# Kernel optimization log

Measured on AMD Instinct MI355X. Metric: run time of the kernel, lower is better.

## Reference

```python
import jax, jax.numpy as jnp
import numpy as np

N_NODES = 50000
N_EDGES = 800000
IN_C, H0, H1, OUT_C = 64, 64, 64, 16
EPS = 1e-5


def _sage_min(x, src, dst, Wl, bl, Wr, n_nodes):
    # PyG SAGEConv(aggr='min'): out = lin_l(min_{j in N(i)} x_j) + lin_r(x_i)
    agg = jax.ops.segment_min(x[src], dst, num_segments=n_nodes)
    agg = jnp.where(jnp.isfinite(agg), agg, 0.0)  # empty segments -> 0 (torch_scatter default)
    return agg @ Wl + bl + x @ Wr


def _batchnorm(x, gamma, beta):
    # training-mode BatchNorm1d over node dim, biased variance, eps=1e-5
    mu = jnp.mean(x, axis=0)
    var = jnp.mean((x - mu) ** 2, axis=0)
    return gamma * (x - mu) * jax.lax.rsqrt(var + EPS) + beta


def setup_inputs() -> dict:
    key = jax.random.key(0)
    ks = jax.random.split(key, 16)
    x = jax.random.normal(ks[0], (N_NODES, IN_C), dtype=jnp.float32)
    edge_index = jax.random.randint(ks[1], (2, N_EDGES), 0, N_NODES, dtype=jnp.int64)

    def lin(k, fan_in, fan_out):
        s = 1.0 / np.sqrt(fan_in)
        return jax.random.uniform(k, (fan_in, fan_out), jnp.float32, -s, s)

    return {
        "x": x, "edge_index": edge_index,
        "W1l": lin(ks[2], IN_C, H0), "b1": jnp.zeros((H0,), jnp.float32), "W1r": lin(ks[3], IN_C, H0),
        "g1": jnp.ones((H0,), jnp.float32), "be1": jnp.zeros((H0,), jnp.float32),
        "W2l": lin(ks[4], H0, H1), "b2": jnp.zeros((H1,), jnp.float32), "W2r": lin(ks[5], H0, H1),
        "g2": jnp.ones((H1,), jnp.float32), "be2": jnp.zeros((H1,), jnp.float32),
        "W3l": lin(ks[6], H1, OUT_C), "b3": jnp.zeros((OUT_C,), jnp.float32), "W3r": lin(ks[7], H1, OUT_C),
    }


def reference(x, edge_index, W1l, b1, W1r, g1, be1, W2l, b2, W2r, g2, be2, W3l, b3, W3r):
    src, dst = edge_index[0], edge_index[1]
    n = x.shape[0]
    h = jax.nn.relu(_batchnorm(_sage_min(x, src, dst, W1l, b1, W1r, n), g1, be1))
    h = jax.nn.relu(_batchnorm(_sage_min(h, src, dst, W2l, b2, W2r, n), g2, be2))
    h = _sage_min(h, src, dst, W3l, b3, W3r, n)
    return jax.nn.log_softmax(h, axis=1)
```

## Files before the change

kernel.cpp:

```cpp
#include <hip/hip_runtime.h>
#include <stdint.h>


#define NG 8

__device__ __forceinline__ float bnrelu1(float v, float mu, float is, float g, float b) {
    return fmaxf((v - mu) * is * g + b, 0.0f);
}

__global__ __launch_bounds__(256)
void k_prep(int* __restrict__ deg, int n_nodes, const int* __restrict__ ei32,
            int* __restrict__ flag) {
    int i = blockIdx.x * blockDim.x + threadIdx.x;
    int stride = gridDim.x * blockDim.x;
    for (int j = i; j < n_nodes; j += stride) deg[j] = 0;
    if (i == 0) {
        int allzero = 1;
        for (int t = 1; t < 32; t += 2) allzero &= (ei32[t] == 0);
        *flag = allzero;
    }
}

__global__ __launch_bounds__(256)
void k_convert(const void* __restrict__ ei, int n_edges,
               const int* __restrict__ flag, int* __restrict__ src32,
               int* __restrict__ dst32) {
    const bool is64 = (*flag != 0);
    const int* e32 = (const int*)ei;
    const long long* e64 = (const long long*)ei;
    int i = blockIdx.x * blockDim.x + threadIdx.x;
    int stride = gridDim.x * blockDim.x;
    for (int e = i; e < n_edges; e += stride) {
        if (is64) { src32[e] = (int)e64[e]; dst32[e] = (int)e64[n_edges + e]; }
        else      { src32[e] = e32[e];      dst32[e] = e32[n_edges + e]; }
    }
}

__global__ __launch_bounds__(256)
void k_hist_r(const int* __restrict__ dst32, int n_edges, int* __restrict__ deg,
              int NN, int blocks_per_group) {
    const int g = blockIdx.x & (NG - 1);
    const int jb = blockIdx.x >> 3;
    const int lo = (int)((long long)g * NN / NG);
    const int hi = (int)((long long)(g + 1) * NN / NG);
    const int stride = blocks_per_group * 256;
    for (int e = jb * 256 + threadIdx.x; e < n_edges; e += stride) {
        int d = dst32[e];
        if (d >= lo && d < hi) atomicAdd(&deg[d], 1);
    }
}

__global__ __launch_bounds__(256)
void k_scan1(const int* __restrict__ deg, int* __restrict__ bsum, int n) {
    __shared__ int red[256];
    const int t = threadIdx.x;
    const int i = blockIdx.x * 256 + t;
    red[t] = (i < n) ? deg[i] : 0;
    __syncthreads();
    for (int off = 128; off; off >>= 1) {
        if (t < off) red[t] += red[t + off];
        __syncthreads();
    }
    if (t == 0) bsum[blockIdx.x] = red[0];
}

__global__ __launch_bounds__(1024)
void k_scan2(const int* __restrict__ bsum, int* __restrict__ boffs,
             int nb, int* __restrict__ rowptr, int n) {
    __shared__ int part[1024];
    const int t = threadIdx.x;
    part[t] = (t < nb) ? bsum[t] : 0;
    __syncthreads();
    for (int off = 1; off < 1024; off <<= 1) {
        int v = (t >= off) ? part[t - off] : 0;
        __syncthreads();
        part[t] += v;
        __syncthreads();
    }
    if (t < nb) boffs[t] = (t == 0) ? 0 : part[t - 1];
    if (t == 0) rowptr[n] = part[nb - 1];
}

__global__ __launch_bounds__(256)
void k_scan3(const int* __restrict__ deg, const int* __restrict__ boffs,
             int* __restrict__ rowptr, int* __restrict__ cursor, int n) {
    __shared__ int part[256];
    const int t = threadIdx.x;
    const int i = blockIdx.x * 256 + t;
    const int d = (i < n) ? deg[i] : 0;
    part[t] = d;
    __syncthreads();
    for (int off = 1; off < 256; off <<= 1) {
        int v = (t >= off) ? part[t - off] : 0;
        __syncthreads();
        part[t] += v;
        __syncthreads();
    }
    if (i < n) {
        int excl = boffs[blockIdx.x] + part[t] - d;
        rowptr[i] = excl;
        cursor[i] = excl;
    }
}

__global__ __launch_bounds__(256)
void k_fill_r(const int* __restrict__ src32, const int* __restrict__ dst32,
              int n_edges, int* __restrict__ cursor, int* __restrict__ csr,
              int NN, int blocks_per_group) {
    const int g = blockIdx.x & (NG - 1);
    const int jb = blockIdx.x >> 3;
    const int lo = (int)((long long)g * NN / NG);
    const int hi = (int)((long long)(g + 1) * NN / NG);
    const int stride = blocks_per_group * 256;
    for (int e = jb * 256 + threadIdx.x; e < n_edges; e += stride) {
        int d = dst32[e];
        if (d >= lo && d < hi) {
            int pos = atomicAdd(&cursor[d], 1);
            csr[pos] = src32[e];
        }
    }
}

template <bool BN>
__global__ __launch_bounds__(256)
void k_agg(const float* __restrict__ x, const int* __restrict__ rowptr,
           const int* __restrict__ csr, float* __restrict__ agg, int NN,
           const float* __restrict__ mu, const float* __restrict__ istd,
           const float* __restrict__ gam, const float* __restrict__ bet) {
    const int lane = threadIdx.x & 63;
    const int wave = (blockIdx.x * blockDim.x + threadIdx.x) >> 6;
    const int nwaves = (gridDim.x * blockDim.x) >> 6;
    float s_mu = 0.f, s_is = 0.f, s_g = 0.f, s_b = 0.f;
    if (BN) { s_mu = mu[lane]; s_is = istd[lane]; s_g = gam[lane]; s_b = bet[lane]; }
    for (int n = wave; n < NN; n += nwaves) {
        const int beg = rowptr[n], end = rowptr[n + 1];
        float m = __builtin_inff();
        int e = beg;
        for (; e + 4 <= end; e += 4) {
            int s0 = csr[e], s1 = csr[e + 1], s2 = csr[e + 2], s3 = csr[e + 3];
            float v0 = x[(size_t)s0 * 64 + lane];
            float v1 = x[(size_t)s1 * 64 + lane];
            float v2 = x[(size_t)s2 * 64 + lane];
            float v3 = x[(size_t)s3 * 64 + lane];
            if (BN) {
                v0 = bnrelu1(v0, s_mu, s_is, s_g, s_b);
                v1 = bnrelu1(v1, s_mu, s_is, s_g, s_b);
                v2 = bnrelu1(v2, s_mu, s_is, s_g, s_b);
                v3 = bnrelu1(v3, s_mu, s_is, s_g, s_b);
            }
            m = fminf(m, fminf(fminf(v0, v1), fminf(v2, v3)));
        }
        for (; e < end; ++e) {
            float v = x[(size_t)csr[e] * 64 + lane];
            if (BN) v = bnrelu1(v, s_mu, s_is, s_g, s_b);
            m = fminf(m, v);
        }
        agg[(size_t)n * 64 + lane] = (end > beg) ? m : 0.0f;
    }
}

template <bool BNX>
__global__ __launch_bounds__(256)
void k_gemm64(const float* __restrict__ agg, const float* __restrict__ xin,
              const float* __restrict__ Wl, const float* __restrict__ bl,
              const float* __restrict__ Wr, float* __restrict__ hout,
              double* __restrict__ psum, double* __restrict__ psq, int n_nodes,
              const float* __restrict__ mu, const float* __restrict__ istd,
              const float* __restrict__ gam, const float* __restrict__ bet) {
    __shared__ float sWl[64][64];
    __shared__ float sWr[64][64];
    __shared__ float rowA[4][64];
    __shared__ float rowX[4][64];
    __shared__ double red[4][64];
    const int t = threadIdx.x, c = t & 63, ln = t >> 6;
    for (int i = t; i < 4096; i += 256) {
        ((float*)sWl)[i] = Wl[i];
        ((float*)sWr)[i] = Wr[i];
    }
    float s_mu = 0.f, s_is = 0.f, s_g = 0.f, s_b = 0.f;
    if (BNX) { s_mu = mu[c]; s_is = istd[c]; s_g = gam[c]; s_b = bet[c]; }
    const float bc = bl[c];
    double lsum = 0.0, lsq = 0.0;
    const int nchunk = (n_nodes + 3) >> 2;
    for (int chunk = blockIdx.x; chunk < nchunk; chunk += gridDim.x) {
        const int node = chunk * 4 + ln;
        __syncthreads();
        if (node < n_nodes) {
            rowA[ln][c] = agg[(size_t)node * 64 + c];
            float v = xin[(size_t)node * 64 + c];
            if (BNX) v = bnrelu1(v, s_mu, s_is, s_g, s_b);
            rowX[ln][c] = v;
        }
        __syncthreads();
        if (node < n_nodes) {
            float acc = bc;
#pragma unroll
            for (int k = 0; k < 64; ++k)
                acc = fmaf(rowA[ln][k], sWl[k][c], fmaf(rowX[ln][k], sWr[k][c], acc));
            hout[(size_t)node * 64 + c] = acc;
            lsum += (double)acc;
            lsq  += (double)acc * (double)acc;
        }
    }
    __syncthreads();
    red[ln][c] = lsum;
    __syncthreads();
    if (ln == 0)
        psum[(size_t)blockIdx.x * 64 + c] = red[0][c] + red[1][c] + red[2][c] + red[3][c];
    __syncthreads();
    red[ln][c] = lsq;
    __syncthreads();
    if (ln == 0)
        psq[(size_t)blockIdx.x * 64 + c] = red[0][c] + red[1][c] + red[2][c] + red[3][c];
}

__global__ __launch_bounds__(1024)
void k_finalize(const double* __restrict__ psum, const double* __restrict__ psq,
                float* __restrict__ mu, float* __restrict__ istd,
                int n_nodes, int nblocks) {
    __shared__ double s_s[16][64];
    __shared__ double s_q[16][64];
    const int t = threadIdx.x;
    const int c = t & 63, g = t >> 6;
    double s = 0.0, q = 0.0;
    for (int b = g; b < nblocks; b += 16) {
        s += psum[(size_t)b * 64 + c];
        q += psq[(size_t)b * 64 + c];
    }
    s_s[g][c] = s;
    s_q[g][c] = q;
    __syncthreads();
    if (g == 0) {
        double S = 0.0, Q = 0.0;
#pragma unroll
        for (int i = 0; i < 16; ++i) { S += s_s[i][c]; Q += s_q[i][c]; }
        double m = S / n_nodes;
        double var = Q / n_nodes - m * m;
        mu[c] = (float)m;
        istd[c] = (float)(1.0 / sqrt(var + 1e-5));
    }
}

__global__ __launch_bounds__(256)
void k_l3(const float* __restrict__ agg, const float* __restrict__ xin,
          const float* __restrict__ W3l, const float* __restrict__ b3,
          const float* __restrict__ W3r, float* __restrict__ out, int n_nodes,
          const float* __restrict__ mu, const float* __restrict__ istd,
          const float* __restrict__ gam, const float* __restrict__ bet) {
    __shared__ float sWl[64][16];
    __shared__ float sWr[64][16];
    __shared__ float rowA[16][65];
    __shared__ float rowX[16][65];
    const int t = threadIdx.x;
    for (int i = t; i < 1024; i += 256) {
        ((float*)sWl)[i] = W3l[i];
        ((float*)sWr)[i] = W3r[i];
    }
    const int kc = t & 63;
    const float s_mu = mu[kc], s_is = istd[kc], s_g = gam[kc], s_b = bet[kc];
    const int base = blockIdx.x * 16;
#pragma unroll
    for (int i = 0; i < 4; ++i) {
        int j = t + i * 256;
        int nd = j >> 6, k = j & 63;
        int gnode = base + nd;
        if (gnode < n_nodes) {
            rowA[nd][k] = agg[(size_t)gnode * 64 + k];
            rowX[nd][k] = bnrelu1(xin[(size_t)gnode * 64 + k], s_mu, s_is, s_g, s_b);
        } else {
            rowA[nd][k] = 0.0f;
            rowX[nd][k] = 0.0f;
        }
    }
    __syncthreads();
    const int n = t >> 4, c = t & 15;
    float acc = b3[c];
#pragma unroll
    for (int k = 0; k < 64; ++k)
        acc = fmaf(rowA[n][k], sWl[k][c], fmaf(rowX[n][k], sWr[k][c], acc));
    float m = acc;
    for (int off = 8; off; off >>= 1) m = fmaxf(m, __shfl_xor(m, off, 16));
    float ex = expf(acc - m);
    float ssum = ex;
    for (int off = 8; off; off >>= 1) ssum += __shfl_xor(ssum, off, 16);
    if (base + n < n_nodes)
        out[(size_t)(base + n) * 16 + c] = (acc - m) - logf(ssum);
}

extern "C" void kernel_launch(void* const* d_in, const int* in_sizes, int n_in,
                              void* d_out, int out_size, void* d_ws, size_t ws_size,
                              hipStream_t stream) {
    (void)n_in; (void)out_size; (void)ws_size;
    const float* x   = (const float*)d_in[0];
    const void*  ei  = d_in[1];
    const float* W1l = (const float*)d_in[2];
    const float* b1  = (const float*)d_in[3];
    const float* W1r = (const float*)d_in[4];
    const float* g1  = (const float*)d_in[5];
    const float* be1 = (const float*)d_in[6];
    const float* W2l = (const float*)d_in[7];
    const float* b2  = (const float*)d_in[8];
    const float* W2r = (const float*)d_in[9];
    const float* g2  = (const float*)d_in[10];
    const float* be2 = (const float*)d_in[11];
    const float* W3l = (const float*)d_in[12];
    const float* b3  = (const float*)d_in[13];
    const float* W3r = (const float*)d_in[14];
    float* out = (float*)d_out;

    const int NN = in_sizes[0] / 64;
    const int n_edges = in_sizes[1] / 2;
    const int nAgg = NN * 64;

    size_t off = 0;
    auto alloc = [&](size_t bytes) {
        void* p = (char*)d_ws + off;
        off = (off + bytes + 255) & ~(size_t)255;
        return p;
    };
    float* agg    = (float*)alloc((size_t)nAgg * 4);
    float* hA     = (float*)alloc((size_t)nAgg * 4);
    float* hB     = (float*)alloc((size_t)nAgg * 4);
    int*   csr    = (int*)  alloc((size_t)n_edges * 4);
    int*   src32  = (int*)  alloc((size_t)n_edges * 4);
    int*   dst32  = (int*)  alloc((size_t)n_edges * 4);
    int*   rowptr = (int*)  alloc((size_t)(NN + 1) * 4);
    int*   cursor = (int*)  alloc((size_t)NN * 4);
    int*   deg    = (int*)  alloc((size_t)NN * 4);
    int*   bsum   = (int*)  alloc(1024 * 4);
    int*   boffs  = (int*)  alloc(1024 * 4);
    const int GG = 512;
    double* psum  = (double*)alloc((size_t)GG * 64 * 8);
    double* psq   = (double*)alloc((size_t)GG * 64 * 8);
    float*  mu1   = (float*) alloc(64 * 4);
    float*  istd1 = (float*) alloc(64 * 4);
    float*  mu2   = (float*) alloc(64 * 4);
    float*  istd2 = (float*) alloc(64 * 4);
    int*    flag  = (int*)   alloc(4);

    const int GHF = 1024;
    const int BPG = GHF / NG;
    const int NB = (NN + 255) / 256;
    const int GA = 2048;
    const int GL3 = (NN + 15) / 16;

    k_prep   <<<256, 256, 0, stream>>>(deg, NN, (const int*)ei, flag);
    k_convert<<<1024, 256, 0, stream>>>(ei, n_edges, flag, src32, dst32);
    k_hist_r <<<GHF, 256, 0, stream>>>(dst32, n_edges, deg, NN, BPG);
    k_scan1  <<<NB, 256, 0, stream>>>(deg, bsum, NN);
    k_scan2  <<<1, 1024, 0, stream>>>(bsum, boffs, NB, rowptr, NN);
    k_scan3  <<<NB, 256, 0, stream>>>(deg, boffs, rowptr, cursor, NN);
    k_fill_r <<<GHF, 256, 0, stream>>>(src32, dst32, n_edges, cursor, csr, NN, BPG);

    k_agg<false><<<GA, 256, 0, stream>>>(x, rowptr, csr, agg, NN,
                                         nullptr, nullptr, nullptr, nullptr);
    k_gemm64<false><<<GG, 256, 0, stream>>>(agg, x, W1l, b1, W1r, hA, psum, psq, NN,
                                            nullptr, nullptr, nullptr, nullptr);
    k_finalize<<<1, 1024, 0, stream>>>(psum, psq, mu1, istd1, NN, GG);
    k_agg<true><<<GA, 256, 0, stream>>>(hA, rowptr, csr, agg, NN, mu1, istd1, g1, be1);
    k_gemm64<true><<<GG, 256, 0, stream>>>(agg, hA, W2l, b2, W2r, hB, psum, psq, NN,
                                           mu1, istd1, g1, be1);
    k_finalize<<<1, 1024, 0, stream>>>(psum, psq, mu2, istd2, NN, GG);
    k_agg<true><<<GA, 256, 0, stream>>>(hB, rowptr, csr, agg, NN, mu2, istd2, g2, be2);
    k_l3<<<GL3, 256, 0, stream>>>(agg, hB, W3l, b3, W3r, out, NN, mu2, istd2, g2, be2);
}
```

Baseline: 404.6 us.

## Fuse min-aggregation with per-node linear layers and merge histogram into conversion

Merges the gather-min aggregation and the dense Wl/Wr projection into a single per-layer kernel. Each wave aggregates one node, stages the row in shared memory, and multiplies it against weights held in registers. This removes the intermediate agg buffer round-trip and several launches, and the final layer is fused the same way including log-softmax. The degree histogram is folded into the index-conversion kernel with plain global atomics, dropping the grouped pass. BN partial sums move from double to float accumulation, and the 128 weight registers per thread may limit occupancy.

```diff
diff --git a/kernel.cpp b/kernel.cpp
--- a/kernel.cpp
+++ b/kernel.cpp
@@ -22,31 +22,21 @@
 }
 
 __global__ __launch_bounds__(256)
-void k_convert(const void* __restrict__ ei, int n_edges,
-               const int* __restrict__ flag, int* __restrict__ src32,
-               int* __restrict__ dst32) {
+void k_convert_hist(const void* __restrict__ ei, int n_edges,
+                    const int* __restrict__ flag, int* __restrict__ src32,
+                    int* __restrict__ dst32, int* __restrict__ deg) {
     const bool is64 = (*flag != 0);
     const int* e32 = (const int*)ei;
     const long long* e64 = (const long long*)ei;
     int i = blockIdx.x * blockDim.x + threadIdx.x;
     int stride = gridDim.x * blockDim.x;
     for (int e = i; e < n_edges; e += stride) {
-        if (is64) { src32[e] = (int)e64[e]; dst32[e] = (int)e64[n_edges + e]; }
-        else      { src32[e] = e32[e];      dst32[e] = e32[n_edges + e]; }
-    }
-}
-
-__global__ __launch_bounds__(256)
-void k_hist_r(const int* __restrict__ dst32, int n_edges, int* __restrict__ deg,
-              int NN, int blocks_per_group) {
-    const int g = blockIdx.x & (NG - 1);
-    const int jb = blockIdx.x >> 3;
-    const int lo = (int)((long long)g * NN / NG);
-    const int hi = (int)((long long)(g + 1) * NN / NG);
-    const int stride = blocks_per_group * 256;
-    for (int e = jb * 256 + threadIdx.x; e < n_edges; e += stride) {
-        int d = dst32[e];
-        if (d >= lo && d < hi) atomicAdd(&deg[d], 1);
+        int s, d;
+        if (is64) { s = (int)e64[e]; d = (int)e64[n_edges + e]; }
+        else      { s = e32[e];      d = e32[n_edges + e]; }
+        src32[e] = s;
+        dst32[e] = d;
+        atomicAdd(&deg[d], 1);
     }
 }
 
@@ -122,100 +112,105 @@
 }
 
 template <bool BN>
-__global__ __launch_bounds__(256)
-void k_agg(const float* __restrict__ x, const int* __restrict__ rowptr,
-           const int* __restrict__ csr, float* __restrict__ agg, int NN,
-           const float* __restrict__ mu, const float* __restrict__ istd,
-           const float* __restrict__ gam, const float* __restrict__ bet) {
-    const int lane = threadIdx.x & 63;
-    const int wave = (blockIdx.x * blockDim.x + threadIdx.x) >> 6;
-    const int nwaves = (gridDim.x * blockDim.x) >> 6;
+__global__ __launch_bounds__(256, 2)
+void k_layer(const float* __restrict__ xin, const int* __restrict__ rowptr,
+             const int* __restrict__ csr, const float* __restrict__ Wl,
+             const float* __restrict__ bl, const float* __restrict__ Wr,
+             float* __restrict__ hout, float* __restrict__ psum,
+             float* __restrict__ psq, int NN,
+             const float* __restrict__ mu, const float* __restrict__ istd,
+             const float* __restrict__ gam, const float* __restrict__ bet) {
+    __shared__ float rowA[4][64];
+    __shared__ float rowX[4][64];
+    __shared__ float red[4][64];
+    const int t = threadIdx.x, lane = t & 63, w = t >> 6;
+    float wl[64], wr[64];
+#pragma unroll
+    for (int k = 0; k < 64; ++k) {
+        wl[k] = Wl[k * 64 + lane];
+        wr[k] = Wr[k * 64 + lane];
+    }
     float s_mu = 0.f, s_is = 0.f, s_g = 0.f, s_b = 0.f;
     if (BN) { s_mu = mu[lane]; s_is = istd[lane]; s_g = gam[lane]; s_b = bet[lane]; }
+    const float bc = bl[lane];
+    float lsum = 0.f, lsq = 0.f;
+    const int wave = blockIdx.x * 4 + w;
+    const int nwaves = gridDim.x * 4;
     for (int n = wave; n < NN; n += nwaves) {
         const int beg = rowptr[n], end = rowptr[n + 1];
         float m = __builtin_inff();
         int e = beg;
-        for (; e + 4 <= end; e += 4) {
+        for (; e + 8 <= end; e += 8) {
             int s0 = csr[e], s1 = csr[e + 1], s2 = csr[e + 2], s3 = csr[e + 3];
-            float v0 = x[(size_t)s0 * 64 + lane];
-            float v1 = x[(size_t)s1 * 64 + lane];
-            float v2 = x[(size_t)s2 * 64 + lane];
-            float v3 = x[(size_t)s3 * 64 + lane];
+            int s4 = csr[e + 4], s5 = csr[e + 5], s6 = csr[e + 6], s7 = csr[e + 7];
+            float v0 = xin[(size_t)s0 * 64 + lane];
+            float v1 = xin[(size_t)s1 * 64 + lane];
+            float v2 = xin[(size_t)s2 * 64 + lane];
+            float v3 = xin[(size_t)s3 * 64 + lane];
+            float v4 = xin[(size_t)s4 * 64 + lane];
+            float v5 = xin[(size_t)s5 * 64 + lane];
+            float v6 = xin[(size_t)s6 * 64 + lane];
+            float v7 = xin[(size_t)s7 * 64 + lane];
             if (BN) {
                 v0 = bnrelu1(v0, s_mu, s_is, s_g, s_b);
                 v1 = bnrelu1(v1, s_mu, s_is, s_g, s_b);
                 v2 = bnrelu1(v2, s_mu, s_is, s_g, s_b);
                 v3 = bnrelu1(v3, s_mu, s_is, s_g, s_b);
+                v4 = bnrelu1(v4, s_mu, s_is, s_g, s_b);
+                v5 = bnrelu1(v5, s_mu, s_is, s_g, s_b);
+                v6 = bnrelu1(v6, s_mu, s_is, s_g, s_b);
+                v7 = bnrelu1(v7, s_mu, s_is, s_g, s_b);
             }
-            m = fminf(m, fminf(fminf(v0, v1), fminf(v2, v3)));
+            m = fminf(m, fminf(fminf(fminf(v0, v1), fminf(v2, v3)),
+                               fminf(fminf(v4, v5), fminf(v6, v7))));
         }
         for (; e < end; ++e) {
-            float v = x[(size_t)csr[e] * 64 + lane];
+            float v = xin[(size_t)csr[e] * 64 + lane];
             if (BN) v = bnrelu1(v, s_mu, s_is, s_g, s_b);
             m = fminf(m, v);
         }
-        agg[(size_t)n * 64 + lane] = (end > beg) ? m : 0.0f;
-    }
-}
-
-template <bool BNX>
-__global__ __launch_bounds__(256)
-void k_gemm64(const float* __restrict__ agg, const float* __restrict__ xin,
-              const float* __restrict__ Wl, const float* __restrict__ bl,
-              const float* __restrict__ Wr, float* __restrict__ hout,
-              double* __restrict__ psum, double* __restrict__ psq, int n_nodes,
-              const float* __restrict__ mu, const float* __restrict__ istd,
-              const float* __restrict__ gam, const float* __restrict__ bet) {
-    __shared__ float sWl[64][64];
-    __shared__ float sWr[64][64];
-    __shared__ float rowA[4][64];
-    __shared__ float rowX[4][64];
-    __shared__ double red[4][64];
-    const int t = threadIdx.x, c = t & 63, ln = t >> 6;
-    for (int i = t; i < 4096; i += 256) {
-        ((float*)sWl)[i] = Wl[i];
-        ((float*)sWr)[i] = Wr[i];
-    }
-    float s_mu = 0.f, s_is = 0.f, s_g = 0.f, s_b = 0.f;
-    if (BNX) { s_mu = mu[c]; s_is = istd[c]; s_g = gam[c]; s_b = bet[c]; }
-    const float bc = bl[c];
-    double lsum = 0.0, lsq = 0.0;
-    const int nchunk = (n_nodes + 3) >> 2;
-    for (int chunk = blockIdx.x; chunk < nchunk; chunk += gridDim.x) {
-        const int node = chunk * 4 + ln;
-        __syncthreads();
-        if (node < n_nodes) {
-            rowA[ln][c] = agg[(size_t)node * 64 + c];
-            float v = xin[(size_t)node * 64 + c];
-            if (BNX) v = bnrelu1(v, s_mu, s_is, s_g, s_b);
-            rowX[ln][c] = v;
-        }
-        __syncthreads();
-        if (node < n_nodes) {
-            float acc = bc;
-#pragma unroll
-            for (int k = 0; k < 64; ++k)
-                acc = fmaf(rowA[ln][k], sWl[k][c], fmaf(rowX[ln][k], sWr[k][c], acc));
-            hout[(size_t)node * 64 + c] = acc;
-            lsum += (double)acc;
-            lsq  += (double)acc * (double)acc;
-        }
-    }
-    __syncthreads();
-    red[ln][c] = lsum;
-    __syncthreads();
-    if (ln == 0)
-        psum[(size_t)blockIdx.x * 64 + c] = red[0][c] + red[1][c] + red[2][c] + red[3][c];
-    __syncthreads();
-    red[ln][c] = lsq;
-    __syncthreads();
-    if (ln == 0)
-        psq[(size_t)blockIdx.x * 64 + c] = red[0][c] + red[1][c] + red[2][c] + red[3][c];
+        const float av = (end > beg) ? m : 0.0f;
+        float xv = xin[(size_t)n * 64 + lane];
+        if (BN) xv = bnrelu1(xv, s_mu, s_is, s_g, s_b);
+        rowA[w][lane] = av;
+        rowX[w][lane] = xv;
+        asm volatile("s_waitcnt lgkmcnt(0)" ::: "memory");
+        __builtin_amdgcn_sched_barrier(0);
+        float a0 = 0.f, a1 = 0.f, a2 = 0.f, a3 = 0.f;
+#pragma unroll
+        for (int k4 = 0; k4 < 16; ++k4) {
+            const float4 a4 = *(const float4*)&rowA[w][k4 * 4];
+            const float4 x4 = *(const float4*)&rowX[w][k4 * 4];
+            a0 = fmaf(a4.x, wl[k4 * 4 + 0], a0);
+            a1 = fmaf(a4.y, wl[k4 * 4 + 1], a1);
+            a2 = fmaf(a4.z, wl[k4 * 4 + 2], a2);
+            a3 = fmaf(a4.w, wl[k4 * 4 + 3], a3);
+            a0 = fmaf(x4.x, wr[k4 * 4 + 0], a0);
+            a1 = fmaf(x4.y, wr[k4 * 4 + 1], a1);
+            a2 = fmaf(x4.z, wr[k4 * 4 + 2], a2);
+            a3 = fmaf(x4.w, wr[k4 * 4 + 3], a3);
+        }
+        const float h = bc + ((a0 + a1) + (a2 + a3));
+        hout[(size_t)n * 64 + lane] = h;
+        lsum += h;
+        lsq = fmaf(h, h, lsq);
+    }
+    __syncthreads();
+    red[w][lane] = lsum;
+    __syncthreads();
+    if (w == 0)
+        psum[(size_t)blockIdx.x * 64 + lane] =
+            red[0][lane] + red[1][lane] + red[2][lane] + red[3][lane];
+    __syncthreads();
+    red[w][lane] = lsq;
+    __syncthreads();
+    if (w == 0)
+        psq[(size_t)blockIdx.x * 64 + lane] =
+            red[0][lane] + red[1][lane] + red[2][lane] + red[3][lane];
 }
 
 __global__ __launch_bounds__(1024)
-void k_finalize(const double* __restrict__ psum, const double* __restrict__ psq,
+void k_finalize(const float* __restrict__ psum, const float* __restrict__ psq,
                 float* __restrict__ mu, float* __restrict__ istd,
                 int n_nodes, int nblocks) {
     __shared__ double s_s[16][64];
@@ -224,8 +219,8 @@
     const int c = t & 63, g = t >> 6;
     double s = 0.0, q = 0.0;
     for (int b = g; b < nblocks; b += 16) {
-        s += psum[(size_t)b * 64 + c];
-        q += psq[(size_t)b * 64 + c];
+        s += (double)psum[(size_t)b * 64 + c];
+        q += (double)psq[(size_t)b * 64 + c];
     }
     s_s[g][c] = s;
     s_q[g][c] = q;
@@ -241,50 +236,76 @@
     }
 }
 
-__global__ __launch_bounds__(256)
-void k_l3(const float* __restrict__ agg, const float* __restrict__ xin,
-          const float* __restrict__ W3l, const float* __restrict__ b3,
-          const float* __restrict__ W3r, float* __restrict__ out, int n_nodes,
-          const float* __restrict__ mu, const float* __restrict__ istd,
-          const float* __restrict__ gam, const float* __restrict__ bet) {
-    __shared__ float sWl[64][16];
-    __shared__ float sWr[64][16];
-    __shared__ float rowA[16][65];
-    __shared__ float rowX[16][65];
-    const int t = threadIdx.x;
-    for (int i = t; i < 1024; i += 256) {
-        ((float*)sWl)[i] = W3l[i];
-        ((float*)sWr)[i] = W3r[i];
-    }
-    const int kc = t & 63;
-    const float s_mu = mu[kc], s_is = istd[kc], s_g = gam[kc], s_b = bet[kc];
-    const int base = blockIdx.x * 16;
-#pragma unroll
-    for (int i = 0; i < 4; ++i) {
-        int j = t + i * 256;
-        int nd = j >> 6, k = j & 63;
-        int gnode = base + nd;
-        if (gnode < n_nodes) {
-            rowA[nd][k] = agg[(size_t)gnode * 64 + k];
-            rowX[nd][k] = bnrelu1(xin[(size_t)gnode * 64 + k], s_mu, s_is, s_g, s_b);
-        } else {
-            rowA[nd][k] = 0.0f;
-            rowX[nd][k] = 0.0f;
-        }
-    }
-    __syncthreads();
-    const int n = t >> 4, c = t & 15;
-    float acc = b3[c];
-#pragma unroll
-    for (int k = 0; k < 64; ++k)
-        acc = fmaf(rowA[n][k], sWl[k][c], fmaf(rowX[n][k], sWr[k][c], acc));
-    float m = acc;
-    for (int off = 8; off; off >>= 1) m = fmaxf(m, __shfl_xor(m, off, 16));
-    float ex = expf(acc - m);
-    float ssum = ex;
-    for (int off = 8; off; off >>= 1) ssum += __shfl_xor(ssum, off, 16);
-    if (base + n < n_nodes)
-        out[(size_t)(base + n) * 16 + c] = (acc - m) - logf(ssum);
+__global__ __launch_bounds__(256, 2)
+void k_layer3(const float* __restrict__ xin, const int* __restrict__ rowptr,
+              const int* __restrict__ csr, const float* __restrict__ W3l,
+              const float* __restrict__ b3, const float* __restrict__ W3r,
+              float* __restrict__ out, int NN,
+              const float* __restrict__ mu, const float* __restrict__ istd,
+              const float* __restrict__ gam, const float* __restrict__ bet) {
+    __shared__ float rowA[4][64];
+    __shared__ float rowX[4][64];
+    const int t = threadIdx.x, lane = t & 63, w = t >> 6;
+    const int c = lane & 15, q = lane >> 4;
+    float wl3[16], wr3[16];
+#pragma unroll
+    for (int j = 0; j < 16; ++j) {
+        wl3[j] = W3l[(q * 16 + j) * 16 + c];
+        wr3[j] = W3r[(q * 16 + j) * 16 + c];
+    }
+    const float s_mu = mu[lane], s_is = istd[lane], s_g = gam[lane], s_b = bet[lane];
+    const float bc = b3[c];
+    const int wave = blockIdx.x * 4 + w;
+    const int nwaves = gridDim.x * 4;
+    for (int n = wave; n < NN; n += nwaves) {
+        const int beg = rowptr[n], end = rowptr[n + 1];
+        float m = __builtin_inff();
+        int e = beg;
+        for (; e + 8 <= end; e += 8) {
+            int s0 = csr[e], s1 = csr[e + 1], s2 = csr[e + 2], s3 = csr[e + 3];
+            int s4 = csr[e + 4], s5 = csr[e + 5], s6 = csr[e + 6], s7 = csr[e + 7];
+            float v0 = bnrelu1(xin[(size_t)s0 * 64 + lane], s_mu, s_is, s_g, s_b);
+            float v1 = bnrelu1(xin[(size_t)s1 * 64 + lane], s_mu, s_is, s_g, s_b);
+            float v2 = bnrelu1(xin[(size_t)s2 * 64 + lane], s_mu, s_is, s_g, s_b);
+            float v3 = bnrelu1(xin[(size_t)s3 * 64 + lane], s_mu, s_is, s_g, s_b);
+            float v4 = bnrelu1(xin[(size_t)s4 * 64 + lane], s_mu, s_is, s_g, s_b);
+            float v5 = bnrelu1(xin[(size_t)s5 * 64 + lane], s_mu, s_is, s_g, s_b);
+            float v6 = bnrelu1(xin[(size_t)s6 * 64 + lane], s_mu, s_is, s_g, s_b);
+            float v7 = bnrelu1(xin[(size_t)s7 * 64 + lane], s_mu, s_is, s_g, s_b);
+            m = fminf(m, fminf(fminf(fminf(v0, v1), fminf(v2, v3)),
+                               fminf(fminf(v4, v5), fminf(v6, v7))));
+        }
+        for (; e < end; ++e)
+            m = fminf(m, bnrelu1(xin[(size_t)csr[e] * 64 + lane], s_mu, s_is, s_g, s_b));
+        rowA[w][lane] = (end > beg) ? m : 0.0f;
+        rowX[w][lane] = bnrelu1(xin[(size_t)n * 64 + lane], s_mu, s_is, s_g, s_b);
+        asm volatile("s_waitcnt lgkmcnt(0)" ::: "memory");
+        __builtin_amdgcn_sched_barrier(0);
+        float p0 = 0.f, p1 = 0.f;
+#pragma unroll
+        for (int j4 = 0; j4 < 4; ++j4) {
+            const float4 a4 = *(const float4*)&rowA[w][q * 16 + j4 * 4];
+            const float4 x4 = *(const float4*)&rowX[w][q * 16 + j4 * 4];
+            p0 = fmaf(a4.x, wl3[j4 * 4 + 0], p0);
+            p1 = fmaf(a4.y, wl3[j4 * 4 + 1], p1);
+            p0 = fmaf(a4.z, wl3[j4 * 4 + 2], p0);
+            p1 = fmaf(a4.w, wl3[j4 * 4 + 3], p1);
+            p0 = fmaf(x4.x, wr3[j4 * 4 + 0], p0);
+            p1 = fmaf(x4.y, wr3[j4 * 4 + 1], p1);
+            p0 = fmaf(x4.z, wr3[j4 * 4 + 2], p0);
+            p1 = fmaf(x4.w, wr3[j4 * 4 + 3], p1);
+        }
+        float acc = p0 + p1;
+        acc += __shfl_xor(acc, 16);
+        acc += __shfl_xor(acc, 32);
+        acc += bc;
+        float mx = acc;
+        for (int off = 8; off; off >>= 1) mx = fmaxf(mx, __shfl_xor(mx, off, 16));
+        float ex = expf(acc - mx);
+        float ss = ex;
+        for (int off = 8; off; off >>= 1) ss += __shfl_xor(ss, off, 16);
+        if (lane < 16) out[(size_t)n * 16 + c] = (acc - mx) - logf(ss);
+    }
 }
 
 extern "C" void kernel_launch(void* const* d_in, const int* in_sizes, int n_in,
@@ -318,7 +339,6 @@
         off = (off + bytes + 255) & ~(size_t)255;
         return p;
     };
-    float* agg    = (float*)alloc((size_t)nAgg * 4);
     float* hA     = (float*)alloc((size_t)nAgg * 4);
     float* hB     = (float*)alloc((size_t)nAgg * 4);
     int*   csr    = (int*)  alloc((size_t)n_edges * 4);
@@ -329,38 +349,33 @@
     int*   deg    = (int*)  alloc((size_t)NN * 4);
     int*   bsum   = (int*)  alloc(1024 * 4);
     int*   boffs  = (int*)  alloc(1024 * 4);
-    const int GG = 512;
-    double* psum  = (double*)alloc((size_t)GG * 64 * 8);
-    double* psq   = (double*)alloc((size_t)GG * 64 * 8);
-    float*  mu1   = (float*) alloc(64 * 4);
-    float*  istd1 = (float*) alloc(64 * 4);
-    float*  mu2   = (float*) alloc(64 * 4);
-    float*  istd2 = (float*) alloc(64 * 4);
-    int*    flag  = (int*)   alloc(4);
+    const int GL = 768;
+    float* psum   = (float*)alloc((size_t)GL * 64 * 4);
+    float* psq    = (float*)alloc((size_t)GL * 64 * 4);
+    float* mu1    = (float*)alloc(64 * 4);
+    float* istd1  = (float*)alloc(64 * 4);
+    float* mu2    = (float*)alloc(64 * 4);
+    float* istd2  = (float*)alloc(64 * 4);
+    int*   flag   = (int*)  alloc(4);
 
     const int GHF = 1024;
     const int BPG = GHF / NG;
     const int NB = (NN + 255) / 256;
-    const int GA = 2048;
-    const int GL3 = (NN + 15) / 16;
-
-    k_prep   <<<256, 256, 0, stream>>>(deg, NN, (const int*)ei, flag);
-    k_convert<<<1024, 256, 0, stream>>>(ei, n_edges, flag, src32, dst32);
-    k_hist_r <<<GHF, 256, 0, stream>>>(dst32, n_edges, deg, NN, BPG);
-    k_scan1  <<<NB, 256, 0, stream>>>(deg, bsum, NN);
-    k_scan2  <<<1, 1024, 0, stream>>>(bsum, boffs, NB, rowptr, NN);
-    k_scan3  <<<NB, 256, 0, stream>>>(deg, boffs, rowptr, cursor, NN);
-    k_fill_r <<<GHF, 256, 0, stream>>>(src32, dst32, n_edges, cursor, csr, NN, BPG);
-
-    k_agg<false><<<GA, 256, 0, stream>>>(x, rowptr, csr, agg, NN,
-                                         nullptr, nullptr, nullptr, nullptr);
-    k_gemm64<false><<<GG, 256, 0, stream>>>(agg, x, W1l, b1, W1r, hA, psum, psq, NN,
-                                            nullptr, nullptr, nullptr, nullptr);
-    k_finalize<<<1, 1024, 0, stream>>>(psum, psq, mu1, istd1, NN, GG);
-    k_agg<true><<<GA, 256, 0, stream>>>(hA, rowptr, csr, agg, NN, mu1, istd1, g1, be1);
-    k_gemm64<true><<<GG, 256, 0, stream>>>(agg, hA, W2l, b2, W2r, hB, psum, psq, NN,
-                                           mu1, istd1, g1, be1);
-    k_finalize<<<1, 1024, 0, stream>>>(psum, psq, mu2, istd2, NN, GG);
-    k_agg<true><<<GA, 256, 0, stream>>>(hB, rowptr, csr, agg, NN, mu2, istd2, g2, be2);
-    k_l3<<<GL3, 256, 0, stream>>>(agg, hB, W3l, b3, W3r, out, NN, mu2, istd2, g2, be2);
-}
+
+    k_prep        <<<256, 256, 0, stream>>>(deg, NN, (const int*)ei, flag);
+    k_convert_hist<<<1024, 256, 0, stream>>>(ei, n_edges, flag, src32, dst32, deg);
+    k_scan1       <<<NB, 256, 0, stream>>>(deg, bsum, NN);
+    k_scan2       <<<1, 1024, 0, stream>>>(bsum, boffs, NB, rowptr, NN);
+    k_scan3       <<<NB, 256, 0, stream>>>(deg, boffs, rowptr, cursor, NN);
+    k_fill_r      <<<GHF, 256, 0, stream>>>(src32, dst32, n_edges, cursor, csr, NN, BPG);
+
+    k_layer<false><<<GL, 256, 0, stream>>>(x, rowptr, csr, W1l, b1, W1r, hA,
+                                           psum, psq, NN,
+                                           nullptr, nullptr, nullptr, nullptr);
+    k_finalize<<<1, 1024, 0, stream>>>(psum, psq, mu1, istd1, NN, GL);
+    k_layer<true><<<GL, 256, 0, stream>>>(hA, rowptr, csr, W2l, b2, W2r, hB,
+                                          psum, psq, NN, mu1, istd1, g1, be1);
+    k_finalize<<<1, 1024, 0, stream>>>(psum, psq, mu2, istd2, NN, GL);
+    k_layer3<<<GL, 256, 0, stream>>>(hB, rowptr, csr, W3l, b3, W3r, out, NN,
+                                     mu2, istd2, g2, be2);
+}
```

Measured after the change: 490.2 us. 1.21x slower.

## Register-tile the layer GEMM and fuse edge conversion with degree histogram

Applied to the files above, without the earlier changes.

Replaces the one-output-per-thread GEMM with a 64-node tile in which each thread computes a 4x4 register block using float4 weight loads from shared memory. BN partial sums move from double to float per block, and one block now covers each 64-node tile. The int64-to-int32 edge conversion also does the degree atomics directly, which drops the separate range-partitioned histogram pass. This gives up the locality of grouped atomics and some partial-sum precision in return for fewer launches and more arithmetic per shared-memory load.

```diff
diff --git a/kernel.cpp b/kernel.cpp
--- a/kernel.cpp
+++ b/kernel.cpp
@@ -22,31 +22,21 @@
 }
 
 __global__ __launch_bounds__(256)
-void k_convert(const void* __restrict__ ei, int n_edges,
-               const int* __restrict__ flag, int* __restrict__ src32,
-               int* __restrict__ dst32) {
+void k_convert_hist(const void* __restrict__ ei, int n_edges,
+                    const int* __restrict__ flag, int* __restrict__ src32,
+                    int* __restrict__ dst32, int* __restrict__ deg) {
     const bool is64 = (*flag != 0);
     const int* e32 = (const int*)ei;
     const long long* e64 = (const long long*)ei;
     int i = blockIdx.x * blockDim.x + threadIdx.x;
     int stride = gridDim.x * blockDim.x;
     for (int e = i; e < n_edges; e += stride) {
-        if (is64) { src32[e] = (int)e64[e]; dst32[e] = (int)e64[n_edges + e]; }
-        else      { src32[e] = e32[e];      dst32[e] = e32[n_edges + e]; }
-    }
-}
-
-__global__ __launch_bounds__(256)
-void k_hist_r(const int* __restrict__ dst32, int n_edges, int* __restrict__ deg,
-              int NN, int blocks_per_group) {
-    const int g = blockIdx.x & (NG - 1);
-    const int jb = blockIdx.x >> 3;
-    const int lo = (int)((long long)g * NN / NG);
-    const int hi = (int)((long long)(g + 1) * NN / NG);
-    const int stride = blocks_per_group * 256;
-    for (int e = jb * 256 + threadIdx.x; e < n_edges; e += stride) {
-        int d = dst32[e];
-        if (d >= lo && d < hi) atomicAdd(&deg[d], 1);
+        int s, d;
+        if (is64) { s = (int)e64[e]; d = (int)e64[n_edges + e]; }
+        else      { s = e32[e];      d = e32[n_edges + e]; }
+        src32[e] = s;
+        dst32[e] = d;
+        atomicAdd(&deg[d], 1);
     }
 }
 
@@ -161,61 +151,124 @@
 
 template <bool BNX>
 __global__ __launch_bounds__(256)
-void k_gemm64(const float* __restrict__ agg, const float* __restrict__ xin,
-              const float* __restrict__ Wl, const float* __restrict__ bl,
-              const float* __restrict__ Wr, float* __restrict__ hout,
-              double* __restrict__ psum, double* __restrict__ psq, int n_nodes,
-              const float* __restrict__ mu, const float* __restrict__ istd,
-              const float* __restrict__ gam, const float* __restrict__ bet) {
+void k_gemm64t(const float* __restrict__ agg, const float* __restrict__ xin,
+               const float* __restrict__ Wl, const float* __restrict__ bl,
+               const float* __restrict__ Wr, float* __restrict__ hout,
+               float* __restrict__ psum, float* __restrict__ psq, int NN,
+               const float* __restrict__ mu, const float* __restrict__ istd,
+               const float* __restrict__ gam, const float* __restrict__ bet) {
     __shared__ float sWl[64][64];
     __shared__ float sWr[64][64];
-    __shared__ float rowA[4][64];
-    __shared__ float rowX[4][64];
-    __shared__ double red[4][64];
-    const int t = threadIdx.x, c = t & 63, ln = t >> 6;
-    for (int i = t; i < 4096; i += 256) {
-        ((float*)sWl)[i] = Wl[i];
-        ((float*)sWr)[i] = Wr[i];
-    }
-    float s_mu = 0.f, s_is = 0.f, s_g = 0.f, s_b = 0.f;
-    if (BNX) { s_mu = mu[c]; s_is = istd[c]; s_g = gam[c]; s_b = bet[c]; }
-    const float bc = bl[c];
-    double lsum = 0.0, lsq = 0.0;
-    const int nchunk = (n_nodes + 3) >> 2;
-    for (int chunk = blockIdx.x; chunk < nchunk; chunk += gridDim.x) {
-        const int node = chunk * 4 + ln;
-        __syncthreads();
-        if (node < n_nodes) {
-            rowA[ln][c] = agg[(size_t)node * 64 + c];
-            float v = xin[(size_t)node * 64 + c];
-            if (BNX) v = bnrelu1(v, s_mu, s_is, s_g, s_b);
-            rowX[ln][c] = v;
-        }
-        __syncthreads();
-        if (node < n_nodes) {
-            float acc = bc;
-#pragma unroll
-            for (int k = 0; k < 64; ++k)
-                acc = fmaf(rowA[ln][k], sWl[k][c], fmaf(rowX[ln][k], sWr[k][c], acc));
-            hout[(size_t)node * 64 + c] = acc;
-            lsum += (double)acc;
-            lsq  += (double)acc * (double)acc;
-        }
-    }
-    __syncthreads();
-    red[ln][c] = lsum;
-    __syncthreads();
-    if (ln == 0)
-        psum[(size_t)blockIdx.x * 64 + c] = red[0][c] + red[1][c] + red[2][c] + red[3][c];
-    __syncthreads();
-    red[ln][c] = lsq;
-    __syncthreads();
-    if (ln == 0)
-        psq[(size_t)blockIdx.x * 64 + c] = red[0][c] + red[1][c] + red[2][c] + red[3][c];
+    __shared__ float rowA[64][68];
+    __shared__ float rowX[64][68];
+    __shared__ float4 red4[4][64];
+    const int t = threadIdx.x;
+#pragma unroll
+    for (int i = 0; i < 4; ++i) {
+        int id = i * 256 + t;
+        ((float4*)sWl)[id] = ((const float4*)Wl)[id];
+        ((float4*)sWr)[id] = ((const float4*)Wr)[id];
+    }
+    const int base = blockIdx.x * 64;
+#pragma unroll
+    for (int i = 0; i < 4; ++i) {
+        int id = i * 256 + t;
+        int n = id >> 4, s = id & 15;
+        int gn = base + n;
+        float4 a4 = {0.f, 0.f, 0.f, 0.f};
+        float4 x4 = {0.f, 0.f, 0.f, 0.f};
+        if (gn < NN) {
+            a4 = *(const float4*)&agg[(size_t)gn * 64 + s * 4];
+            x4 = *(const float4*)&xin[(size_t)gn * 64 + s * 4];
+            if (BNX) {
+                const float4 m4 = *(const float4*)&mu[s * 4];
+                const float4 i4 = *(const float4*)&istd[s * 4];
+                const float4 g4 = *(const float4*)&gam[s * 4];
+                const float4 b4 = *(const float4*)&bet[s * 4];
+                x4.x = bnrelu1(x4.x, m4.x, i4.x, g4.x, b4.x);
+                x4.y = bnrelu1(x4.y, m4.y, i4.y, g4.y, b4.y);
+                x4.z = bnrelu1(x4.z, m4.z, i4.z, g4.z, b4.z);
+                x4.w = bnrelu1(x4.w, m4.w, i4.w, g4.w, b4.w);
+            }
+        }
+        *(float4*)&rowA[n][s * 4] = a4;
+        *(float4*)&rowX[n][s * 4] = x4;
+    }
+    __syncthreads();
+    const int lane = t & 63, w = t >> 6;
+    const int cg = lane & 15, ng = lane >> 4;
+    const int c0 = cg * 4;
+    const int nb = w * 16 + ng * 4;
+    float4 acc[4];
+#pragma unroll
+    for (int j = 0; j < 4; ++j) acc[j] = {0.f, 0.f, 0.f, 0.f};
+#pragma unroll
+    for (int k = 0; k < 64; ++k) {
+        const float4 wl4 = *(const float4*)&sWl[k][c0];
+        const float4 wr4 = *(const float4*)&sWr[k][c0];
+#pragma unroll
+        for (int j = 0; j < 4; ++j) {
+            const float a = rowA[nb + j][k];
+            const float xv = rowX[nb + j][k];
+            acc[j].x = fmaf(a, wl4.x, acc[j].x);
+            acc[j].y = fmaf(a, wl4.y, acc[j].y);
+            acc[j].z = fmaf(a, wl4.z, acc[j].z);
+            acc[j].w = fmaf(a, wl4.w, acc[j].w);
+            acc[j].x = fmaf(xv, wr4.x, acc[j].x);
+            acc[j].y = fmaf(xv, wr4.y, acc[j].y);
+            acc[j].z = fmaf(xv, wr4.z, acc[j].z);
+            acc[j].w = fmaf(xv, wr4.w, acc[j].w);
+        }
+    }
+    const float4 bc4 = *(const float4*)&bl[c0];
+    float4 ls = {0.f, 0.f, 0.f, 0.f};
+    float4 lq = {0.f, 0.f, 0.f, 0.f};
+#pragma unroll
+    for (int j = 0; j < 4; ++j) {
+        const int gn = base + nb + j;
+        if (gn < NN) {
+            float4 h;
+            h.x = bc4.x + acc[j].x;
+            h.y = bc4.y + acc[j].y;
+            h.z = bc4.z + acc[j].z;
+            h.w = bc4.w + acc[j].w;
+            *(float4*)&hout[(size_t)gn * 64 + c0] = h;
+            ls.x += h.x; ls.y += h.y; ls.z += h.z; ls.w += h.w;
+            lq.x = fmaf(h.x, h.x, lq.x);
+            lq.y = fmaf(h.y, h.y, lq.y);
+            lq.z = fmaf(h.z, h.z, lq.z);
+            lq.w = fmaf(h.w, h.w, lq.w);
+        }
+    }
+    red4[w][lane] = ls;
+    __syncthreads();
+    if (t < 64) {
+        const int rcg = t >> 2, comp = t & 3;
+        float S = 0.f;
+#pragma unroll
+        for (int ww = 0; ww < 4; ++ww)
+#pragma unroll
+            for (int g = 0; g < 4; ++g)
+                S += ((const float*)&red4[ww][g * 16 + rcg])[comp];
+        psum[(size_t)blockIdx.x * 64 + t] = S;
+    }
+    __syncthreads();
+    red4[w][lane] = lq;
+    __syncthreads();
+    if (t < 64) {
+        const int rcg = t >> 2, comp = t & 3;
+        float S = 0.f;
+#pragma unroll
+        for (int ww = 0; ww < 4; ++ww)
+#pragma unroll
+            for (int g = 0; g < 4; ++g)
+                S += ((const float*)&red4[ww][g * 16 + rcg])[comp];
+        psq[(size_t)blockIdx.x * 64 + t] = S;
+    }
 }
 
 __global__ __launch_bounds__(1024)
-void k_finalize(const double* __restrict__ psum, const double* __restrict__ psq,
+void k_finalize(const float* __restrict__ psum, const float* __restrict__ psq,
                 float* __restrict__ mu, float* __restrict__ istd,
                 int n_nodes, int nblocks) {
     __shared__ double s_s[16][64];
@@ -224,8 +277,8 @@
     const int c = t & 63, g = t >> 6;
     double s = 0.0, q = 0.0;
     for (int b = g; b < nblocks; b += 16) {
-        s += psum[(size_t)b * 64 + c];
-        q += psq[(size_t)b * 64 + c];
+        s += (double)psum[(size_t)b * 64 + c];
+        q += (double)psq[(size_t)b * 64 + c];
     }
     s_s[g][c] = s;
     s_q[g][c] = q;
@@ -329,14 +382,14 @@
     int*   deg    = (int*)  alloc((size_t)NN * 4);
     int*   bsum   = (int*)  alloc(1024 * 4);
     int*   boffs  = (int*)  alloc(1024 * 4);
-    const int GG = 512;
-    double* psum  = (double*)alloc((size_t)GG * 64 * 8);
-    double* psq   = (double*)alloc((size_t)GG * 64 * 8);
-    float*  mu1   = (float*) alloc(64 * 4);
-    float*  istd1 = (float*) alloc(64 * 4);
-    float*  mu2   = (float*) alloc(64 * 4);
-    float*  istd2 = (float*) alloc(64 * 4);
-    int*    flag  = (int*)   alloc(4);
+    const int NB64 = (NN + 63) / 64;
+    float* psum   = (float*)alloc((size_t)NB64 * 64 * 4);
+    float* psq    = (float*)alloc((size_t)NB64 * 64 * 4);
+    float* mu1    = (float*)alloc(64 * 4);
+    float* istd1  = (float*)alloc(64 * 4);
+    float* mu2    = (float*)alloc(64 * 4);
+    float* istd2  = (float*)alloc(64 * 4);
+    int*   flag   = (int*)  alloc(4);
 
     const int GHF = 1024;
     const int BPG = GHF / NG;
@@ -344,23 +397,23 @@
     const int GA = 2048;
     const int GL3 = (NN + 15) / 16;
 
-    k_prep   <<<256, 256, 0, stream>>>(deg, NN, (const int*)ei, flag);
-    k_convert<<<1024, 256, 0, stream>>>(ei, n_edges, flag, src32, dst32);
-    k_hist_r <<<GHF, 256, 0, stream>>>(dst32, n_edges, deg, NN, BPG);
-    k_scan1  <<<NB, 256, 0, stream>>>(deg, bsum, NN);
-    k_scan2  <<<1, 1024, 0, stream>>>(bsum, boffs, NB, rowptr, NN);
-    k_scan3  <<<NB, 256, 0, stream>>>(deg, boffs, rowptr, cursor, NN);
-    k_fill_r <<<GHF, 256, 0, stream>>>(src32, dst32, n_edges, cursor, csr, NN, BPG);
+    k_prep        <<<256, 256, 0, stream>>>(deg, NN, (const int*)ei, flag);
+    k_convert_hist<<<1024, 256, 0, stream>>>(ei, n_edges, flag, src32, dst32, deg);
+    k_scan1       <<<NB, 256, 0, stream>>>(deg, bsum, NN);
+    k_scan2       <<<1, 1024, 0, stream>>>(bsum, boffs, NB, rowptr, NN);
+    k_scan3       <<<NB, 256, 0, stream>>>(deg, boffs, rowptr, cursor, NN);
+    k_fill_r      <<<GHF, 256, 0, stream>>>(src32, dst32, n_edges, cursor, csr, NN, BPG);
 
     k_agg<false><<<GA, 256, 0, stream>>>(x, rowptr, csr, agg, NN,
                                          nullptr, nullptr, nullptr, nullptr);
-    k_gemm64<false><<<GG, 256, 0, stream>>>(agg, x, W1l, b1, W1r, hA, psum, psq, NN,
-                                            nullptr, nullptr, nullptr, nullptr);
-    k_finalize<<<1, 1024, 0, stream>>>(psum, psq, mu1, istd1, NN, GG);
+    k_gemm64t<false><<<NB64, 256, 0, stream>>>(agg, x, W1l, b1, W1r, hA,
+                                               psum, psq, NN,
+                                               nullptr, nullptr, nullptr, nullptr);
+    k_finalize<<<1, 1024, 0, stream>>>(psum, psq, mu1, istd1, NN, NB64);
     k_agg<true><<<GA, 256, 0, stream>>>(hA, rowptr, csr, agg, NN, mu1, istd1, g1, be1);
-    k_gemm64<true><<<GG, 256, 0, stream>>>(agg, hA, W2l, b2, W2r, hB, psum, psq, NN,
-                                           mu1, istd1, g1, be1);
-    k_finalize<<<1, 1024, 0, stream>>>(psum, psq, mu2, istd2, NN, GG);
+    k_gemm64t<true><<<NB64, 256, 0, stream>>>(agg, hA, W2l, b2, W2r, hB,
+                                              psum, psq, NN, mu1, istd1, g1, be1);
+    k_finalize<<<1, 1024, 0, stream>>>(psum, psq, mu2, istd2, NN, NB64);
     k_agg<true><<<GA, 256, 0, stream>>>(hB, rowptr, csr, agg, NN, mu2, istd2, g2, be2);
     k_l3<<<GL3, 256, 0, stream>>>(agg, hB, W3l, b3, W3r, out, NN, mu2, istd2, g2, be2);
 }
```

Measured after the change: 896.0 us. 121% more time.
